# Kernel optimization log

Hardware: AMD Instinct MI355X
Metric: run time of the kernel (lower is better)

Reference implementation:

```python
import jax, jax.numpy as jnp
import numpy as np

FP8_MAX = 448.0  # max finite value of float8_e4m3fn


def _fp8_quant_dequant(t, scale):
    """Per-tensor static FP8 e4m3fn quantize -> dequantize (simulated real quant)."""
    q = jnp.clip(t / scale, -FP8_MAX, FP8_MAX).astype(jnp.float8_e4m3fn)
    return q.astype(jnp.float32) * scale


def setup_inputs() -> dict:
    key = jax.random.key(0)
    k1, k2, k3 = jax.random.split(key, 3)
    M, K, N = 4096, 4096, 14336  # tokens, in_features, out_features
    x = jax.random.normal(k1, (M, K), jnp.float32)
    weight = jax.random.normal(k2, (N, K), jnp.float32) * 0.02
    bias = jax.random.normal(k3, (N,), jnp.float32) * 0.01
    # static per-tensor calibration scales (amax / fp8_max)
    input_scale = (jnp.max(jnp.abs(x)) / FP8_MAX).reshape(1)
    weight_scale = (jnp.max(jnp.abs(weight)) / FP8_MAX).reshape(1)
    return {"x": x, "weight": weight, "bias": bias,
            "input_scale": input_scale, "weight_scale": weight_scale}


def reference(x, weight, bias, input_scale, weight_scale):
    # QParamsLinear forward: statically quantize input to fp8 e4m3fn with the
    # input quantizer's per-tensor scale, dequantize the fp8 weight with its
    # per-tensor scale, run the GEMM (y = x_dq @ W_dq^T), and add bias.
    s_in = input_scale[0]
    s_w = weight_scale[0]
    x_dq = _fp8_quant_dequant(x, s_in)      # [M, K]
    w_dq = _fp8_quant_dequant(weight, s_w)  # [N, K]
    return jnp.einsum('mk,nk->mn', x_dq, w_dq) + bias[None, :]
```

## Files before the change

### kernel.cpp

```cpp
#include <hip/hip_runtime.h>
#include <stdint.h>

typedef float f32x4 __attribute__((ext_vector_type(4)));
typedef int   i32x8 __attribute__((ext_vector_type(8)));
typedef long  i64x2 __attribute__((ext_vector_type(2)));

#define FP8_MAX_V 448.0f

__device__ __forceinline__ uint32_t pack4_fp8(float a, float b, float c, float d) {
    a = fminf(fmaxf(a, -FP8_MAX_V), FP8_MAX_V);
    b = fminf(fmaxf(b, -FP8_MAX_V), FP8_MAX_V);
    c = fminf(fmaxf(c, -FP8_MAX_V), FP8_MAX_V);
    d = fminf(fmaxf(d, -FP8_MAX_V), FP8_MAX_V);
    int v = 0;
    v = __builtin_amdgcn_cvt_pk_fp8_f32(a, b, v, false);
    v = __builtin_amdgcn_cvt_pk_fp8_f32(c, d, v, true);
    return (uint32_t)v;
}

__global__ void quant_fp8_kernel(const float* __restrict__ in,
                                 uint32_t* __restrict__ out,
                                 const float* __restrict__ scale_ptr,
                                 long long n4) {
    const float s = scale_ptr[0];
    long long i = (long long)blockIdx.x * blockDim.x + threadIdx.x;
    const long long stride = (long long)gridDim.x * blockDim.x;
    const float4* in4 = (const float4*)in;
    for (; i < n4; i += stride) {
        float4 v = in4[i];
        out[i] = pack4_fp8(v.x / s, v.y / s, v.z / s, v.w / s);
    }
}

__global__ __launch_bounds__(256, 3) void gemm_mxfp8_kernel(
    const uint8_t* __restrict__ qA,
    const uint8_t* __restrict__ qB,
    const float* __restrict__ bias,
    const float* __restrict__ s_in_p,
    const float* __restrict__ s_w_p,
    float* __restrict__ C,
    int M, int N, int K) {
    __shared__ uint8_t lsA[128 * 128];
    __shared__ uint8_t lsB[128 * 128];

    const int tid = threadIdx.x;
    const int w   = tid >> 6;
    const int l   = tid & 63;
    const int wr  = w >> 1;
    const int wc  = w & 1;
    const int lr  = l & 15;
    const int lg  = l >> 4;
    const int lsw = lr & 7;

    const int cpx = (int)gridDim.x >> 3;
    const int swz = ((int)blockIdx.x & 7) * cpx + ((int)blockIdx.x >> 3);
    const int bm  = (swz & 31) << 7;
    const int bn  = (swz >> 5) << 7;

    const float outscale = s_in_p[0] * s_w_p[0];
    const int NT = K >> 7;

    const int off0 = (((lg << 1) ^ lsw) << 4);
    const int off1 = off0 ^ 16;

    f32x4 acc[4][4];
#pragma unroll
    for (int mi = 0; mi < 4; ++mi)
#pragma unroll
        for (int ni = 0; ni < 4; ++ni)
            acc[mi][ni] = (f32x4){0.f, 0.f, 0.f, 0.f};

    const int srow = tid >> 3;
    const int sc   = (((tid & 7) ^ (srow & 7)) << 4);
    const uint8_t* sA = qA + (size_t)(bm + srow) * K + sc;
    const uint8_t* sB = qB + (size_t)(bn + srow) * K + sc;
    const int dstw = w << 10;

    union frag { i32x8 v; i64x2 h[2]; };

    for (int kt = 0; kt < NT; ++kt) {
        const int kb = kt << 7;
#pragma unroll
        for (int i = 0; i < 4; ++i) {
            __builtin_amdgcn_global_load_lds(
                (const __attribute__((address_space(1))) void*)(sA + (size_t)(i * 32) * K + kb),
                (__attribute__((address_space(3))) void*)(lsA + i * 4096 + dstw), 16, 0, 0);
        }
#pragma unroll
        for (int i = 0; i < 4; ++i) {
            __builtin_amdgcn_global_load_lds(
                (const __attribute__((address_space(1))) void*)(sB + (size_t)(i * 32) * K + kb),
                (__attribute__((address_space(3))) void*)(lsB + i * 4096 + dstw), 16, 0, 0);
        }
        __syncthreads();

        i32x8 a[4], b[4];
#pragma unroll
        for (int mi = 0; mi < 4; ++mi) {
            const uint8_t* base = lsA + ((wr * 64 + mi * 16 + lr) << 7);
            frag u;
            u.h[0] = *(const i64x2*)(base + off0);
            u.h[1] = *(const i64x2*)(base + off1);
            a[mi] = u.v;
        }
#pragma unroll
        for (int ni = 0; ni < 4; ++ni) {
            const uint8_t* base = lsB + ((wc * 64 + ni * 16 + lr) << 7);
            frag u;
            u.h[0] = *(const i64x2*)(base + off0);
            u.h[1] = *(const i64x2*)(base + off1);
            b[ni] = u.v;
        }
#pragma unroll
        for (int mi = 0; mi < 4; ++mi)
#pragma unroll
            for (int ni = 0; ni < 4; ++ni)
                acc[mi][ni] = __builtin_amdgcn_mfma_scale_f32_16x16x128_f8f6f4(
                    a[mi], b[ni], acc[mi][ni],
                    0, 0,
                    0, 127,
                    0, 127);
        __syncthreads();
    }

    const int crow0 = bm + wr * 64 + (lg << 2);
    const int ccol0 = bn + wc * 64 + lr;
#pragma unroll
    for (int ni = 0; ni < 4; ++ni) {
        const int col = ccol0 + ni * 16;
        const float bv = bias[col];
#pragma unroll
        for (int mi = 0; mi < 4; ++mi) {
            const int row = crow0 + mi * 16;
#pragma unroll
            for (int r = 0; r < 4; ++r)
                C[(size_t)(row + r) * N + col] = acc[mi][ni][r] * outscale + bv;
        }
    }
}

extern "C" void kernel_launch(void* const* d_in, const int* in_sizes, int n_in,
                              void* d_out, int out_size, void* d_ws, size_t ws_size,
                              hipStream_t stream) {
    const float* x    = (const float*)d_in[0];
    const float* wt   = (const float*)d_in[1];
    const float* bias = (const float*)d_in[2];
    const float* s_in = (const float*)d_in[3];
    const float* s_w  = (const float*)d_in[4];
    float* out = (float*)d_out;

    const long long xe = in_sizes[0];
    const long long we = in_sizes[1];
    const int N = in_sizes[2];
    const int K = (int)(we / N);
    const int M = (int)(xe / K);

    uint8_t* qx = (uint8_t*)d_ws;
    uint8_t* qw = qx + xe;

    quant_fp8_kernel<<<2048, 256, 0, stream>>>(x,  (uint32_t*)qx, s_in, xe >> 2);
    quant_fp8_kernel<<<2048, 256, 0, stream>>>(wt, (uint32_t*)qw, s_w,  we >> 2);

    dim3 grid((M / 128) * (N / 128));
    gemm_mxfp8_kernel<<<grid, 256, 0, stream>>>(qx, qw, bias, s_in, s_w, out,
                                                M, N, K);
}
```

Before: 396.5 us.

## Double-buffer LDS tiles to overlap global loads with MFMA compute

```diff
diff --git a/kernel.cpp b/kernel.cpp
--- a/kernel.cpp
+++ b/kernel.cpp
@@ -32,7 +32,7 @@
     }
 }
 
-__global__ __launch_bounds__(256, 3) void gemm_mxfp8_kernel(
+__global__ __launch_bounds__(256, 2) void gemm_mxfp8_kernel(
     const uint8_t* __restrict__ qA,
     const uint8_t* __restrict__ qB,
     const float* __restrict__ bias,
@@ -40,8 +40,7 @@
     const float* __restrict__ s_w_p,
     float* __restrict__ C,
     int M, int N, int K) {
-    __shared__ uint8_t lsA[128 * 128];
-    __shared__ uint8_t lsB[128 * 128];
+    __shared__ uint8_t lds[2 * 32768];
 
     const int tid = threadIdx.x;
     const int w   = tid >> 6;
@@ -76,28 +75,40 @@
     const uint8_t* sB = qB + (size_t)(bn + srow) * K + sc;
     const int dstw = w << 10;
 
+#define STAGE(SLOT, KB) do { \
+    _Pragma("unroll") \
+    for (int i = 0; i < 4; ++i) { \
+        __builtin_amdgcn_global_load_lds( \
+            (const __attribute__((address_space(1))) void*)(sA + (size_t)(i * 32) * K + (KB)), \
+            (__attribute__((address_space(3))) void*)(lds + (SLOT) * 32768 + i * 4096 + dstw), 16, 0, 0); \
+    } \
+    _Pragma("unroll") \
+    for (int i = 0; i < 4; ++i) { \
+        __builtin_amdgcn_global_load_lds( \
+            (const __attribute__((address_space(1))) void*)(sB + (size_t)(i * 32) * K + (KB)), \
+            (__attribute__((address_space(3))) void*)(lds + (SLOT) * 32768 + 16384 + i * 4096 + dstw), 16, 0, 0); \
+    } \
+} while (0)
+
     union frag { i32x8 v; i64x2 h[2]; };
 
-    for (int kt = 0; kt < NT; ++kt) {
-        const int kb = kt << 7;
-#pragma unroll
-        for (int i = 0; i < 4; ++i) {
-            __builtin_amdgcn_global_load_lds(
-                (const __attribute__((address_space(1))) void*)(sA + (size_t)(i * 32) * K + kb),
-                (__attribute__((address_space(3))) void*)(lsA + i * 4096 + dstw), 16, 0, 0);
+    STAGE(0, 0);
+
+    for (int T = 0; T < NT; ++T) {
+        const uint8_t* rb = lds + (T & 1) * 32768;
+        const int Tp = T + 1;
+        if (Tp < NT) {
+            STAGE(Tp & 1, Tp << 7);
+            asm volatile("s_waitcnt vmcnt(8)" ::: "memory");
+        } else {
+            asm volatile("s_waitcnt vmcnt(0)" ::: "memory");
         }
-#pragma unroll
-        for (int i = 0; i < 4; ++i) {
-            __builtin_amdgcn_global_load_lds(
-                (const __attribute__((address_space(1))) void*)(sB + (size_t)(i * 32) * K + kb),
-                (__attribute__((address_space(3))) void*)(lsB + i * 4096 + dstw), 16, 0, 0);
-        }
-        __syncthreads();
+        __builtin_amdgcn_s_barrier();
 
         i32x8 a[4], b[4];
 #pragma unroll
         for (int mi = 0; mi < 4; ++mi) {
-            const uint8_t* base = lsA + ((wr * 64 + mi * 16 + lr) << 7);
+            const uint8_t* base = rb + ((wr * 64 + mi * 16 + lr) << 7);
             frag u;
             u.h[0] = *(const i64x2*)(base + off0);
             u.h[1] = *(const i64x2*)(base + off1);
@@ -105,7 +116,7 @@
         }
 #pragma unroll
         for (int ni = 0; ni < 4; ++ni) {
-            const uint8_t* base = lsB + ((wc * 64 + ni * 16 + lr) << 7);
+            const uint8_t* base = rb + 16384 + ((wc * 64 + ni * 16 + lr) << 7);
             frag u;
             u.h[0] = *(const i64x2*)(base + off0);
             u.h[1] = *(const i64x2*)(base + off1);
@@ -120,7 +131,9 @@
                     0, 0,
                     0, 127,
                     0, 127);
-        __syncthreads();
+        asm volatile("s_waitcnt lgkmcnt(0)" ::: "memory");
+        __builtin_amdgcn_sched_barrier(0);
+        __builtin_amdgcn_s_barrier();
     }
 
     const int crow0 = bm + wr * 64 + (lg << 2);
@@ -137,6 +150,7 @@
                 C[(size_t)(row + r) * N + col] = acc[mi][ni][r] * outscale + bv;
         }
     }
+#undef STAGE
 }
 
 extern "C" void kernel_launch(void* const* d_in, const int* in_sizes, int n_in,
```

After: 415.8 us. 1.05x slower.

## Triple-buffer LDS with 256x128 tiles, 8 waves, and split-phase MFMA scheduling

Applied to the files above, without the earlier changes.

```diff
diff --git a/kernel.cpp b/kernel.cpp
--- a/kernel.cpp
+++ b/kernel.cpp
@@ -32,7 +32,7 @@
     }
 }
 
-__global__ __launch_bounds__(256, 3) void gemm_mxfp8_kernel(
+__global__ __launch_bounds__(512, 2) void gemm_mxfp8_kernel(
     const uint8_t* __restrict__ qA,
     const uint8_t* __restrict__ qB,
     const float* __restrict__ bias,
@@ -40,8 +40,7 @@
     const float* __restrict__ s_w_p,
     float* __restrict__ C,
     int M, int N, int K) {
-    __shared__ uint8_t lsA[128 * 128];
-    __shared__ uint8_t lsB[128 * 128];
+    extern __shared__ uint8_t lds[];
 
     const int tid = threadIdx.x;
     const int w   = tid >> 6;
@@ -54,8 +53,8 @@
 
     const int cpx = (int)gridDim.x >> 3;
     const int swz = ((int)blockIdx.x & 7) * cpx + ((int)blockIdx.x >> 3);
-    const int bm  = (swz & 31) << 7;
-    const int bn  = (swz >> 5) << 7;
+    const int bm  = (swz & 15) << 8;
+    const int bn  = (swz >> 4) << 7;
 
     const float outscale = s_in_p[0] * s_w_p[0];
     const int NT = K >> 7;
@@ -76,51 +75,85 @@
     const uint8_t* sB = qB + (size_t)(bn + srow) * K + sc;
     const int dstw = w << 10;
 
+#define STA(SL, I, KB) \
+    __builtin_amdgcn_global_load_lds( \
+        (const __attribute__((address_space(1))) void*)(sA + (size_t)((I) * 64) * K + (KB)), \
+        (__attribute__((address_space(3))) void*)(lds + (SL) * 49152 + (I) * 8192 + dstw), 16, 0, 0)
+#define STB(SL, I, KB) \
+    __builtin_amdgcn_global_load_lds( \
+        (const __attribute__((address_space(1))) void*)(sB + (size_t)((I) * 64) * K + (KB)), \
+        (__attribute__((address_space(3))) void*)(lds + (SL) * 49152 + 32768 + (I) * 8192 + dstw), 16, 0, 0)
+
     union frag { i32x8 v; i64x2 h[2]; };
 
-    for (int kt = 0; kt < NT; ++kt) {
-        const int kb = kt << 7;
-#pragma unroll
-        for (int i = 0; i < 4; ++i) {
-            __builtin_amdgcn_global_load_lds(
-                (const __attribute__((address_space(1))) void*)(sA + (size_t)(i * 32) * K + kb),
-                (__attribute__((address_space(3))) void*)(lsA + i * 4096 + dstw), 16, 0, 0);
-        }
-#pragma unroll
-        for (int i = 0; i < 4; ++i) {
-            __builtin_amdgcn_global_load_lds(
-                (const __attribute__((address_space(1))) void*)(sB + (size_t)(i * 32) * K + kb),
-                (__attribute__((address_space(3))) void*)(lsB + i * 4096 + dstw), 16, 0, 0);
-        }
-        __syncthreads();
-
-        i32x8 a[4], b[4];
+    STA(0, 0, 0);  STA(0, 1, 0);  STA(0, 2, 0);  STA(0, 3, 0);
+    STB(0, 0, 0);  STB(0, 1, 0);
+    STA(1, 0, 128); STA(1, 1, 128); STA(1, 2, 128); STA(1, 3, 128);
+    STB(1, 0, 128); STB(1, 1, 128);
+    asm volatile("s_waitcnt vmcnt(6)" ::: "memory");
+    __builtin_amdgcn_s_barrier();
+
+    int s = 0;
+    for (int T = 0; T < NT; ++T) {
+        const uint8_t* base = lds + s * 49152;
+        int sp = s + 2; if (sp >= 3) sp -= 3;
+        const int kbp = (T + 2 < NT ? T + 2 : 0) << 7;
+
+        i32x8 a[4], b[2];
+        STA(sp, 0, kbp); STA(sp, 1, kbp); STA(sp, 2, kbp);
 #pragma unroll
         for (int mi = 0; mi < 4; ++mi) {
-            const uint8_t* base = lsA + ((wr * 64 + mi * 16 + lr) << 7);
+            const uint8_t* p = base + ((wr * 64 + mi * 16 + lr) << 7);
             frag u;
-            u.h[0] = *(const i64x2*)(base + off0);
-            u.h[1] = *(const i64x2*)(base + off1);
+            u.h[0] = *(const i64x2*)(p + off0);
+            u.h[1] = *(const i64x2*)(p + off1);
             a[mi] = u.v;
         }
 #pragma unroll
-        for (int ni = 0; ni < 4; ++ni) {
-            const uint8_t* base = lsB + ((wc * 64 + ni * 16 + lr) << 7);
+        for (int ni = 0; ni < 2; ++ni) {
+            const uint8_t* p = base + 32768 + ((wc * 64 + ni * 16 + lr) << 7);
             frag u;
-            u.h[0] = *(const i64x2*)(base + off0);
-            u.h[1] = *(const i64x2*)(base + off1);
+            u.h[0] = *(const i64x2*)(p + off0);
+            u.h[1] = *(const i64x2*)(p + off1);
             b[ni] = u.v;
         }
+        __builtin_amdgcn_s_barrier();
+        asm volatile("s_waitcnt lgkmcnt(0)" ::: "memory");
+        __builtin_amdgcn_sched_barrier(0);
+        __builtin_amdgcn_s_setprio(1);
 #pragma unroll
         for (int mi = 0; mi < 4; ++mi)
 #pragma unroll
-            for (int ni = 0; ni < 4; ++ni)
+            for (int ni = 0; ni < 2; ++ni)
                 acc[mi][ni] = __builtin_amdgcn_mfma_scale_f32_16x16x128_f8f6f4(
-                    a[mi], b[ni], acc[mi][ni],
-                    0, 0,
-                    0, 127,
-                    0, 127);
-        __syncthreads();
+                    a[mi], b[ni], acc[mi][ni], 0, 0, 0, 127, 0, 127);
+        __builtin_amdgcn_s_setprio(0);
+        __builtin_amdgcn_s_barrier();
+
+        STA(sp, 3, kbp); STB(sp, 0, kbp); STB(sp, 1, kbp);
+#pragma unroll
+        for (int ni = 0; ni < 2; ++ni) {
+            const uint8_t* p = base + 32768 + ((wc * 64 + (ni + 2) * 16 + lr) << 7);
+            frag u;
+            u.h[0] = *(const i64x2*)(p + off0);
+            u.h[1] = *(const i64x2*)(p + off1);
+            b[ni] = u.v;
+        }
+        __builtin_amdgcn_s_barrier();
+        asm volatile("s_waitcnt lgkmcnt(0)" ::: "memory");
+        __builtin_amdgcn_sched_barrier(0);
+        __builtin_amdgcn_s_setprio(1);
+#pragma unroll
+        for (int mi = 0; mi < 4; ++mi)
+#pragma unroll
+            for (int ni = 0; ni < 2; ++ni)
+                acc[mi][ni + 2] = __builtin_amdgcn_mfma_scale_f32_16x16x128_f8f6f4(
+                    a[mi], b[ni], acc[mi][ni + 2], 0, 0, 0, 127, 0, 127);
+        __builtin_amdgcn_s_setprio(0);
+        asm volatile("s_waitcnt vmcnt(6)" ::: "memory");
+        __builtin_amdgcn_s_barrier();
+
+        if (++s == 3) s = 0;
     }
 
     const int crow0 = bm + wr * 64 + (lg << 2);
@@ -137,6 +170,8 @@
                 C[(size_t)(row + r) * N + col] = acc[mi][ni][r] * outscale + bv;
         }
     }
+#undef STA
+#undef STB
 }
 
 extern "C" void kernel_launch(void* const* d_in, const int* in_sizes, int n_in,
@@ -161,7 +196,7 @@
     quant_fp8_kernel<<<2048, 256, 0, stream>>>(x,  (uint32_t*)qx, s_in, xe >> 2);
     quant_fp8_kernel<<<2048, 256, 0, stream>>>(wt, (uint32_t*)qw, s_w,  we >> 2);
 
-    dim3 grid((M / 128) * (N / 128));
-    gemm_mxfp8_kernel<<<grid, 256, 0, stream>>>(qx, qw, bias, s_in, s_w, out,
-                                                M, N, K);
-}
+    dim3 grid((M / 256) * (N / 128));
+    gemm_mxfp8_kernel<<<grid, 512, 147456, stream>>>(qx, qw, bias, s_in, s_w,
+                                                     out, M, N, K);
+}
```

New measurement: 398.7 us. No clear change (+0.6%).

## Pre-pack FP8 operands into MFMA fragment layout and load straight to registers

Applied to the files above, without the earlier changes.

```diff
diff --git a/kernel.cpp b/kernel.cpp
--- a/kernel.cpp
+++ b/kernel.cpp
@@ -3,7 +3,6 @@
 
 typedef float f32x4 __attribute__((ext_vector_type(4)));
 typedef int   i32x8 __attribute__((ext_vector_type(8)));
-typedef long  i64x2 __attribute__((ext_vector_type(2)));
 
 #define FP8_MAX_V 448.0f
 
@@ -18,31 +17,33 @@
     return (uint32_t)v;
 }
 
-__global__ void quant_fp8_kernel(const float* __restrict__ in,
-                                 uint32_t* __restrict__ out,
-                                 const float* __restrict__ scale_ptr,
-                                 long long n4) {
+__global__ void quant_pack_kernel(const float* __restrict__ in,
+                                  uint8_t* __restrict__ out,
+                                  const float* __restrict__ scale_ptr,
+                                  uint32_t total4, int K4, int KT) {
     const float s = scale_ptr[0];
-    long long i = (long long)blockIdx.x * blockDim.x + threadIdx.x;
-    const long long stride = (long long)gridDim.x * blockDim.x;
+    uint32_t i = blockIdx.x * blockDim.x + threadIdx.x;
+    const uint32_t stride = gridDim.x * blockDim.x;
     const float4* in4 = (const float4*)in;
-    for (; i < n4; i += stride) {
+    for (; i < total4; i += stride) {
+        const int m  = i / K4;
+        const int k0 = (i - (uint32_t)m * K4) << 2;
         float4 v = in4[i];
-        out[i] = pack4_fp8(v.x / s, v.y / s, v.z / s, v.w / s);
+        const uint32_t q = pack4_fp8(v.x / s, v.y / s, v.z / s, v.w / s);
+        const size_t addr = ((size_t)(m >> 4) * KT + (k0 >> 7)) * 2048
+                          + (((k0 >> 5) & 3) << 9) + ((m & 15) << 5) + (k0 & 31);
+        *(uint32_t*)(out + addr) = q;
     }
 }
 
-__global__ __launch_bounds__(256, 3) void gemm_mxfp8_kernel(
-    const uint8_t* __restrict__ qA,
-    const uint8_t* __restrict__ qB,
+__global__ __launch_bounds__(256, 2) void gemm_pk_kernel(
+    const uint8_t* __restrict__ pA,
+    const uint8_t* __restrict__ pB,
     const float* __restrict__ bias,
     const float* __restrict__ s_in_p,
     const float* __restrict__ s_w_p,
     float* __restrict__ C,
     int M, int N, int K) {
-    __shared__ uint8_t lsA[128 * 128];
-    __shared__ uint8_t lsB[128 * 128];
-
     const int tid = threadIdx.x;
     const int w   = tid >> 6;
     const int l   = tid & 63;
@@ -50,7 +51,6 @@
     const int wc  = w & 1;
     const int lr  = l & 15;
     const int lg  = l >> 4;
-    const int lsw = lr & 7;
 
     const int cpx = (int)gridDim.x >> 3;
     const int swz = ((int)blockIdx.x & 7) * cpx + ((int)blockIdx.x >> 3);
@@ -58,10 +58,10 @@
     const int bn  = (swz >> 5) << 7;
 
     const float outscale = s_in_p[0] * s_w_p[0];
-    const int NT = K >> 7;
+    const int KT = K >> 7;
 
-    const int off0 = (((lg << 1) ^ lsw) << 4);
-    const int off1 = off0 ^ 16;
+    const uint8_t* aBase = pA + ((size_t)((bm >> 4) + wr * 4) * KT) * 2048 + l * 32;
+    const uint8_t* bBase = pB + ((size_t)((bn >> 4) + wc * 4) * KT) * 2048 + l * 32;
 
     f32x4 acc[4][4];
 #pragma unroll
@@ -70,58 +70,37 @@
         for (int ni = 0; ni < 4; ++ni)
             acc[mi][ni] = (f32x4){0.f, 0.f, 0.f, 0.f};
 
-    const int srow = tid >> 3;
-    const int sc   = (((tid & 7) ^ (srow & 7)) << 4);
-    const uint8_t* sA = qA + (size_t)(bm + srow) * K + sc;
-    const uint8_t* sB = qB + (size_t)(bn + srow) * K + sc;
-    const int dstw = w << 10;
+    i32x8 aC[4], bC[4], aN[4], bN[4];
 
-    union frag { i32x8 v; i64x2 h[2]; };
+#define LOADT(AR, BR, KTI) do { \
+    _Pragma("unroll") \
+    for (int q = 0; q < 4; ++q) \
+        AR[q] = *(const i32x8*)(aBase + ((size_t)q * KT + (KTI)) * 2048); \
+    _Pragma("unroll") \
+    for (int q = 0; q < 4; ++q) \
+        BR[q] = *(const i32x8*)(bBase + ((size_t)q * KT + (KTI)) * 2048); \
+} while (0)
 
-    for (int kt = 0; kt < NT; ++kt) {
-        const int kb = kt << 7;
-#pragma unroll
-        for (int i = 0; i < 4; ++i) {
-            __builtin_amdgcn_global_load_lds(
-                (const __attribute__((address_space(1))) void*)(sA + (size_t)(i * 32) * K + kb),
-                (__attribute__((address_space(3))) void*)(lsA + i * 4096 + dstw), 16, 0, 0);
-        }
-#pragma unroll
-        for (int i = 0; i < 4; ++i) {
-            __builtin_amdgcn_global_load_lds(
-                (const __attribute__((address_space(1))) void*)(sB + (size_t)(i * 32) * K + kb),
-                (__attribute__((address_space(3))) void*)(lsB + i * 4096 + dstw), 16, 0, 0);
-        }
-        __syncthreads();
+#define MM(AR, BR) do { \
+    _Pragma("unroll") \
+    for (int mi = 0; mi < 4; ++mi) \
+        _Pragma("unroll") \
+        for (int ni = 0; ni < 4; ++ni) \
+            acc[mi][ni] = __builtin_amdgcn_mfma_scale_f32_16x16x128_f8f6f4( \
+                AR[mi], BR[ni], acc[mi][ni], 0, 0, 0, 127, 0, 127); \
+} while (0)
 
-        i32x8 a[4], b[4];
-#pragma unroll
-        for (int mi = 0; mi < 4; ++mi) {
-            const uint8_t* base = lsA + ((wr * 64 + mi * 16 + lr) << 7);
-            frag u;
-            u.h[0] = *(const i64x2*)(base + off0);
-            u.h[1] = *(const i64x2*)(base + off1);
-            a[mi] = u.v;
-        }
-#pragma unroll
-        for (int ni = 0; ni < 4; ++ni) {
-            const uint8_t* base = lsB + ((wc * 64 + ni * 16 + lr) << 7);
-            frag u;
-            u.h[0] = *(const i64x2*)(base + off0);
-            u.h[1] = *(const i64x2*)(base + off1);
-            b[ni] = u.v;
-        }
-#pragma unroll
-        for (int mi = 0; mi < 4; ++mi)
-#pragma unroll
-            for (int ni = 0; ni < 4; ++ni)
-                acc[mi][ni] = __builtin_amdgcn_mfma_scale_f32_16x16x128_f8f6f4(
-                    a[mi], b[ni], acc[mi][ni],
-                    0, 0,
-                    0, 127,
-                    0, 127);
-        __syncthreads();
+    LOADT(aC, bC, 0);
+    int kt = 0;
+    for (; kt < KT - 2; kt += 2) {
+        LOADT(aN, bN, kt + 1);
+        MM(aC, bC);
+        LOADT(aC, bC, kt + 2);
+        MM(aN, bN);
     }
+    LOADT(aN, bN, KT - 1);
+    MM(aC, bC);
+    MM(aN, bN);
 
     const int crow0 = bm + wr * 64 + (lg << 2);
     const int ccol0 = bn + wc * 64 + lr;
@@ -137,6 +116,8 @@
                 C[(size_t)(row + r) * N + col] = acc[mi][ni][r] * outscale + bv;
         }
     }
+#undef LOADT
+#undef MM
 }
 
 extern "C" void kernel_launch(void* const* d_in, const int* in_sizes, int n_in,
@@ -154,14 +135,18 @@
     const int N = in_sizes[2];
     const int K = (int)(we / N);
     const int M = (int)(xe / K);
+    const int K4 = K >> 2;
+    const int KT = K >> 7;
 
     uint8_t* qx = (uint8_t*)d_ws;
     uint8_t* qw = qx + xe;
 
-    quant_fp8_kernel<<<2048, 256, 0, stream>>>(x,  (uint32_t*)qx, s_in, xe >> 2);
-    quant_fp8_kernel<<<2048, 256, 0, stream>>>(wt, (uint32_t*)qw, s_w,  we >> 2);
+    quant_pack_kernel<<<2048, 256, 0, stream>>>(x,  qx, s_in,
+                                                (uint32_t)(xe >> 2), K4, KT);
+    quant_pack_kernel<<<2048, 256, 0, stream>>>(wt, qw, s_w,
+                                                (uint32_t)(we >> 2), K4, KT);
 
     dim3 grid((M / 128) * (N / 128));
-    gemm_mxfp8_kernel<<<grid, 256, 0, stream>>>(qx, qw, bias, s_in, s_w, out,
-                                                M, N, K);
+    gemm_pk_kernel<<<grid, 256, 0, stream>>>(qx, qw, bias, s_in, s_w, out,
+                                             M, N, K);
 }
```

Result: slower. 483.7 us (+22.0%).
